# Kernel optimization log

Measured on AMD Instinct MI355X. Metric: run time of the kernel, lower is better.

## Reference

```python
import jax, jax.numpy as jnp
import numpy as np

DIM_U1 = 20
DIM_U2 = 20
DZ = 6
BATCH = 4096


def _mlp(x, Wa, ba, Wb, bb, Wc, bc, Wd, bd):
    h = jax.nn.relu(x @ Wa + ba)
    h = jax.nn.relu(h @ Wb + bb)
    h = jax.nn.relu(h @ Wc + bc)
    return h @ Wd + bd


def setup_inputs() -> dict:
    key = jax.random.key(0)
    ks = jax.random.split(key, 9)

    def lin(k, fan_in, fan_out):
        k1, k2 = jax.random.split(k)
        lim = 1.0 / np.sqrt(fan_in)
        W = jax.random.uniform(k1, (fan_in, fan_out), minval=-lim, maxval=lim, dtype=jnp.float32)
        b = jax.random.uniform(k2, (fan_out,), minval=-lim, maxval=lim, dtype=jnp.float32)
        return W, b

    d = {"x": jax.random.normal(ks[0], (BATCH, DIM_U1), dtype=jnp.float32)}
    dims1 = [(3, 16), (16, 32), (32, 16), (16, 1 + DZ * 3)]
    dims2 = [(3, 16), (16, 32), (32, 16), (16, DZ + 5 * DZ * DZ)]
    names = ["a", "b", "c", "d"]
    for j, (fi, fo) in enumerate(dims1):
        W, b = lin(ks[1 + j], fi, fo)
        d["W1" + names[j]] = W
        d["b1" + names[j]] = b
    for j, (fi, fo) in enumerate(dims2):
        W, b = lin(ks[5 + j], fi, fo)
        d["W2" + names[j]] = W
        d["b2" + names[j]] = b
    return d


def reference(x, W1a, b1a, W1b, b1b, W1c, b1c, W1d, b1d,
              W2a, b2a, W2b, b2b, W2c, b2c, W2d, b2d):
    B = x.shape[0]
    # gather local neighbor triples: [B, dim_u1, 3]
    idx = (jnp.arange(DIM_U1)[:, None] + jnp.arange(-1, 2)[None, :]) % DIM_U1
    xl = x[:, idx]
    out1 = _mlp(xl, W1a, b1a, W1b, b1b, W1c, b1c, W1d, b1d)  # [B, 20, 19]
    out2 = _mlp(xl, W2a, b2a, W2b, b2b, W2c, b2c, W2d, b2d)  # [B, 20, 186]

    f1 = out1[:, :, :1]  # [B, 20, 1]

    # banded scatter for g1: [B, dim_u1, dz*dim_u2]
    rows1 = jnp.arange(DIM_U1)[:, None]
    cols1 = (jnp.arange(3 * DZ)[None, :] + (jnp.arange(DIM_U1)[:, None] - 1) * DZ) % (DZ * DIM_U2)
    g1 = jnp.zeros((B, DIM_U1, DZ * DIM_U2), x.dtype).at[:, rows1, cols1].set(out1[:, :, 1:])

    f2 = out2[:, :, :DZ].reshape(B, DZ * DIM_U2, 1)

    # banded scatter for g2: [B, dz*dim_u2, dz*dim_u2]
    rows2 = jnp.arange(DZ * DIM_U2)[:, None]
    base = (jnp.arange(5 * DZ)[None, :] + (jnp.arange(DIM_U2)[:, None] - 2) * DZ) % (DZ * DIM_U2)  # [20, 30]
    cols2 = jnp.repeat(base, DZ, axis=0)  # [120, 30]
    vals2 = out2[:, :, DZ:].reshape(B, DZ * DIM_U2, 5 * DZ)
    g2 = jnp.zeros((B, DZ * DIM_U2, DZ * DIM_U2), x.dtype).at[:, rows2, cols2].set(vals2)

    return (f1, g1, f2, g2)
```

## Files before the change

kernel.cpp:

```cpp
#include <hip/hip_runtime.h>

#define U 20

struct Ptrs { const float* p[16]; };

__launch_bounds__(64)
__global__ void fused(const float* __restrict__ x, Ptrs pt,
                      float* __restrict__ out, int B, int total) {
    const int tid = threadIdx.x;
    const int t   = blockIdx.x * 64 + tid;

    const size_t g1_off = (size_t)B * 20;
    const size_t f2_off = (size_t)B * 2420;
    const size_t g2_off = (size_t)B * 2540;

    {
        int t0  = blockIdx.x * 64;
        int n_t = total - t0; if (n_t > 64) n_t = 64; if (n_t < 0) n_t = 0;
        float4 z4; z4.x = z4.y = z4.z = z4.w = 0.f;
        float4* z1 = reinterpret_cast<float4*>(out + g1_off + (size_t)t0 * 120);
        int c1 = n_t * 30;
        for (int idx = tid; idx < c1; idx += 64) z1[idx] = z4;
        float4* z2 = reinterpret_cast<float4*>(out + g2_off + (size_t)t0 * 720);
        int c2 = n_t * 180;
        for (int idx = tid; idx < c2; idx += 64) z2[idx] = z4;
    }

    const bool live = (t < total);
    const int b = live ? (t / U) : 0;
    const int i = live ? (t - b * U) : 0;

    const float* W1a = pt.p[0];  const float* b1a = pt.p[1];
    const float* W1b = pt.p[2];  const float* b1b = pt.p[3];
    const float* W1c = pt.p[4];  const float* b1c = pt.p[5];
    const float* W1d = pt.p[6];  const float* b1d = pt.p[7];
    const float* W2a = pt.p[8];  const float* b2a = pt.p[9];
    const float* W2b = pt.p[10]; const float* b2b = pt.p[11];
    const float* W2c = pt.p[12]; const float* b2c = pt.p[13];
    const float* W2d = pt.p[14]; const float* b2d = pt.p[15];

    const float* xb = x + (size_t)b * U;
    int im = (i == 0)     ? U - 1 : i - 1;
    int ip = (i == U - 1) ? 0     : i + 1;
    float v0 = xb[im], v1 = xb[i], v2 = xb[ip];

    float h1[16], h2[32], h3[16];
    float o1[19];

    #pragma unroll
    for (int n = 0; n < 16; n++)
        h1[n] = fmaxf(b1a[n] + v0 * W1a[n] + v1 * W1a[16 + n] + v2 * W1a[32 + n], 0.f);

    #pragma unroll
    for (int n = 0; n < 32; n++) h2[n] = b1b[n];
    #pragma unroll
    for (int k = 0; k < 16; k++) {
        float hk = h1[k];
        #pragma unroll
        for (int n = 0; n < 32; n++) h2[n] += hk * W1b[k * 32 + n];
    }
    #pragma unroll
    for (int n = 0; n < 32; n++) h2[n] = fmaxf(h2[n], 0.f);

    #pragma unroll
    for (int n = 0; n < 16; n++) h3[n] = b1c[n];
    #pragma unroll
    for (int k = 0; k < 32; k++) {
        float hk = h2[k];
        #pragma unroll
        for (int n = 0; n < 16; n++) h3[n] += hk * W1c[k * 16 + n];
    }
    #pragma unroll
    for (int n = 0; n < 16; n++) h3[n] = fmaxf(h3[n], 0.f);

    #pragma unroll
    for (int n = 0; n < 19; n++) o1[n] = b1d[n];
    #pragma unroll
    for (int k = 0; k < 16; k++) {
        float hk = h3[k];
        #pragma unroll
        for (int n = 0; n < 19; n++) o1[n] += hk * W1d[k * 19 + n];
    }

    __syncthreads();
    if (!live) return;

    float* g1row  = out + g1_off + (size_t)t * 120;
    float* g2rows = out + g2_off + (size_t)t * 720;

    out[t] = o1[0];
    #pragma unroll
    for (int j = 0; j < 3; j++) {
        int cc = i - 1 + j;
        if (cc < 0)  cc += U;
        if (cc >= U) cc -= U;
        float2* d = reinterpret_cast<float2*>(g1row + cc * 6);
        #pragma unroll
        for (int m = 0; m < 3; m++) {
            float2 v; v.x = o1[1 + j * 6 + 2 * m]; v.y = o1[1 + j * 6 + 2 * m + 1];
            d[m] = v;
        }
    }

    #pragma unroll
    for (int n = 0; n < 16; n++)
        h1[n] = fmaxf(b2a[n] + v0 * W2a[n] + v1 * W2a[16 + n] + v2 * W2a[32 + n], 0.f);

    #pragma unroll
    for (int n = 0; n < 32; n++) h2[n] = b2b[n];
    #pragma unroll
    for (int k = 0; k < 16; k++) {
        float hk = h1[k];
        #pragma unroll
        for (int n = 0; n < 32; n++) h2[n] += hk * W2b[k * 32 + n];
    }
    #pragma unroll
    for (int n = 0; n < 32; n++) h2[n] = fmaxf(h2[n], 0.f);

    #pragma unroll
    for (int n = 0; n < 16; n++) h3[n] = b2c[n];
    #pragma unroll
    for (int k = 0; k < 32; k++) {
        float hk = h2[k];
        #pragma unroll
        for (int n = 0; n < 16; n++) h3[n] += hk * W2c[k * 16 + n];
    }
    #pragma unroll
    for (int n = 0; n < 16; n++) h3[n] = fmaxf(h3[n], 0.f);

    {
        float o2a[6];
        #pragma unroll
        for (int n = 0; n < 6; n++) o2a[n] = b2d[n];
        #pragma unroll
        for (int k = 0; k < 16; k++) {
            float hk = h3[k];
            #pragma unroll
            for (int n = 0; n < 6; n++) o2a[n] += hk * W2d[k * 186 + n];
        }
        float2* d = reinterpret_cast<float2*>(out + f2_off + (size_t)t * 6);
        #pragma unroll
        for (int m = 0; m < 3; m++) {
            float2 v; v.x = o2a[2 * m]; v.y = o2a[2 * m + 1];
            d[m] = v;
        }
    }

    for (int z = 0; z < 6; z++) {
        float o2[30];
        #pragma unroll
        for (int n = 0; n < 30; n++) o2[n] = b2d[6 + z * 30 + n];
        #pragma unroll
        for (int k = 0; k < 16; k++) {
            float hk = h3[k];
            #pragma unroll
            for (int n = 0; n < 30; n++) o2[n] += hk * W2d[k * 186 + 6 + z * 30 + n];
        }
        float* row = g2rows + z * 120;
        #pragma unroll
        for (int j = 0; j < 5; j++) {
            int cc = i - 2 + j;
            if (cc < 0)  cc += U;
            if (cc >= U) cc -= U;
            float2* d = reinterpret_cast<float2*>(row + cc * 6);
            #pragma unroll
            for (int m = 0; m < 3; m++) {
                float2 v; v.x = o2[j * 6 + 2 * m]; v.y = o2[j * 6 + 2 * m + 1];
                d[m] = v;
            }
        }
    }
}

extern "C" void kernel_launch(void* const* d_in, const int* in_sizes, int n_in,
                              void* d_out, int out_size, void* d_ws, size_t ws_size,
                              hipStream_t stream) {
    const float* x = (const float*)d_in[0];
    Ptrs pt;
    for (int a = 0; a < 16; a++) pt.p[a] = (const float*)d_in[1 + a];

    int total = in_sizes[0];
    int B = total / U;

    int blocks = (total + 63) / 64;
    fused<<<blocks, 64, 0, stream>>>(x, pt, (float*)d_out, B, total);
}
```

Measured before the change: 390.8 us.

## Stage banded outputs in shared memory and write them out coalesced

Instead of zero-filling the global g1/g2 regions and then doing scattered float2 writes per thread, each block builds the full 120-float rows in an LDS tile (zeroed in shared memory) and copies them to global memory with coalesced float4 stores. The same staging is applied to f2. This removes the double write (zero fill plus scatter) to global memory and turns strided writes into contiguous ones. In exchange it adds many __syncthreads barriers and 30KB of LDS per 64-thread block, which may limit occupancy.

```diff
diff --git a/kernel.cpp b/kernel.cpp
--- a/kernel.cpp
+++ b/kernel.cpp
@@ -7,26 +7,17 @@
 __launch_bounds__(64)
 __global__ void fused(const float* __restrict__ x, Ptrs pt,
                       float* __restrict__ out, int B, int total) {
+    __shared__ float buf[64 * 120];
     const int tid = threadIdx.x;
-    const int t   = blockIdx.x * 64 + tid;
+    const int t0  = blockIdx.x * 64;
+    const int t   = t0 + tid;
+    const bool live = (t < total);
+    int n_t = total - t0; if (n_t > 64) n_t = 64; if (n_t < 0) n_t = 0;
 
     const size_t g1_off = (size_t)B * 20;
     const size_t f2_off = (size_t)B * 2420;
     const size_t g2_off = (size_t)B * 2540;
 
-    {
-        int t0  = blockIdx.x * 64;
-        int n_t = total - t0; if (n_t > 64) n_t = 64; if (n_t < 0) n_t = 0;
-        float4 z4; z4.x = z4.y = z4.z = z4.w = 0.f;
-        float4* z1 = reinterpret_cast<float4*>(out + g1_off + (size_t)t0 * 120);
-        int c1 = n_t * 30;
-        for (int idx = tid; idx < c1; idx += 64) z1[idx] = z4;
-        float4* z2 = reinterpret_cast<float4*>(out + g2_off + (size_t)t0 * 720);
-        int c2 = n_t * 180;
-        for (int idx = tid; idx < c2; idx += 64) z2[idx] = z4;
-    }
-
-    const bool live = (t < total);
     const int b = live ? (t / U) : 0;
     const int i = live ? (t - b * U) : 0;
 
@@ -44,8 +35,7 @@
     int ip = (i == U - 1) ? 0     : i + 1;
     float v0 = xb[im], v1 = xb[i], v2 = xb[ip];
 
-    float h1[16], h2[32], h3[16];
-    float o1[19];
+    float h1[16], h2[32], h3[16], o1[19];
 
     #pragma unroll
     for (int n = 0; n < 16; n++)
@@ -82,25 +72,29 @@
         for (int n = 0; n < 19; n++) o1[n] += hk * W1d[k * 19 + n];
     }
 
+    if (live) out[t] = o1[0];
+
+    float4* bv = reinterpret_cast<float4*>(buf);
+    float4 z4; z4.x = z4.y = z4.z = z4.w = 0.f;
+    const int c30 = n_t * 30;
+
+    for (int idx = tid; idx < c30; idx += 64) bv[idx] = z4;
     __syncthreads();
-    if (!live) return;
-
-    float* g1row  = out + g1_off + (size_t)t * 120;
-    float* g2rows = out + g2_off + (size_t)t * 720;
-
-    out[t] = o1[0];
-    #pragma unroll
-    for (int j = 0; j < 3; j++) {
-        int cc = i - 1 + j;
-        if (cc < 0)  cc += U;
-        if (cc >= U) cc -= U;
-        float2* d = reinterpret_cast<float2*>(g1row + cc * 6);
+    if (live) {
+        float* row = buf + tid * 120;
         #pragma unroll
-        for (int m = 0; m < 3; m++) {
-            float2 v; v.x = o1[1 + j * 6 + 2 * m]; v.y = o1[1 + j * 6 + 2 * m + 1];
-            d[m] = v;
+        for (int j = 0; j < 3; j++) {
+            int cc = i - 1 + j; if (cc < 0) cc += U; if (cc >= U) cc -= U;
+            #pragma unroll
+            for (int m = 0; m < 6; m++) row[cc * 6 + m] = o1[1 + j * 6 + m];
         }
     }
+    __syncthreads();
+    {
+        float4* g1v = reinterpret_cast<float4*>(out + g1_off + (size_t)t0 * 120);
+        for (int idx = tid; idx < c30; idx += 64) g1v[idx] = bv[idx];
+    }
+    __syncthreads();
 
     #pragma unroll
     for (int n = 0; n < 16; n++)
@@ -128,7 +122,7 @@
     #pragma unroll
     for (int n = 0; n < 16; n++) h3[n] = fmaxf(h3[n], 0.f);
 
-    {
+    if (live) {
         float o2a[6];
         #pragma unroll
         for (int n = 0; n < 6; n++) o2a[n] = b2d[n];
@@ -138,37 +132,48 @@
             #pragma unroll
             for (int n = 0; n < 6; n++) o2a[n] += hk * W2d[k * 186 + n];
         }
-        float2* d = reinterpret_cast<float2*>(out + f2_off + (size_t)t * 6);
         #pragma unroll
-        for (int m = 0; m < 3; m++) {
-            float2 v; v.x = o2a[2 * m]; v.y = o2a[2 * m + 1];
-            d[m] = v;
-        }
+        for (int n = 0; n < 6; n++) buf[tid * 6 + n] = o2a[n];
     }
+    __syncthreads();
+    {
+        float2* f2g = reinterpret_cast<float2*>(out + f2_off + (size_t)t0 * 6);
+        float2* bv2 = reinterpret_cast<float2*>(buf);
+        int c = n_t * 3;
+        for (int idx = tid; idx < c; idx += 64) f2g[idx] = bv2[idx];
+    }
+    __syncthreads();
 
     for (int z = 0; z < 6; z++) {
-        float o2[30];
-        #pragma unroll
-        for (int n = 0; n < 30; n++) o2[n] = b2d[6 + z * 30 + n];
-        #pragma unroll
-        for (int k = 0; k < 16; k++) {
-            float hk = h3[k];
+        for (int idx = tid; idx < c30; idx += 64) bv[idx] = z4;
+        __syncthreads();
+        if (live) {
+            float o2[30];
             #pragma unroll
-            for (int n = 0; n < 30; n++) o2[n] += hk * W2d[k * 186 + 6 + z * 30 + n];
-        }
-        float* row = g2rows + z * 120;
-        #pragma unroll
-        for (int j = 0; j < 5; j++) {
-            int cc = i - 2 + j;
-            if (cc < 0)  cc += U;
-            if (cc >= U) cc -= U;
-            float2* d = reinterpret_cast<float2*>(row + cc * 6);
+            for (int n = 0; n < 30; n++) o2[n] = b2d[6 + z * 30 + n];
             #pragma unroll
-            for (int m = 0; m < 3; m++) {
-                float2 v; v.x = o2[j * 6 + 2 * m]; v.y = o2[j * 6 + 2 * m + 1];
-                d[m] = v;
+            for (int k = 0; k < 16; k++) {
+                float hk = h3[k];
+                #pragma unroll
+                for (int n = 0; n < 30; n++) o2[n] += hk * W2d[k * 186 + 6 + z * 30 + n];
+            }
+            float* row = buf + tid * 120;
+            #pragma unroll
+            for (int j = 0; j < 5; j++) {
+                int cc = i - 2 + j; if (cc < 0) cc += U; if (cc >= U) cc -= U;
+                #pragma unroll
+                for (int m = 0; m < 6; m++) row[cc * 6 + m] = o2[j * 6 + m];
             }
         }
+        __syncthreads();
+        for (int idx = tid; idx < c30; idx += 64) {
+            int tau = idx / 30;
+            int c   = idx - tau * 30;
+            float4* dst = reinterpret_cast<float4*>(
+                out + g2_off + (size_t)(t0 + tau) * 720 + z * 120 + c * 4);
+            *dst = bv[idx];
+        }
+        __syncthreads();
     }
 }
 
```

New measurement: 391.6 us. Within noise of the previous version (+0.2%).

## Stage MLP weights in LDS and zero output rows per thread

Applied to the files above, without the earlier changes.

All weights and biases are copied into shared memory at block start, with W2d padded to a 188 stride for aligned float2 reads. The hidden layer of width 32 is spilled to a per-thread LDS row instead of registers. The cooperative block-wide zero fill is replaced by each thread zeroing its own g1/g2 rows right before its banded writes. Inner loops are partially rolled to reduce register pressure. This trades repeated global and scalar weight loads for a per-block LDS staging cost of about 23KB plus LDS traffic. The per-thread zero fill gives strided, less coalesced stores and then rewrites the same lines with the banded values.

```diff
diff --git a/kernel.cpp b/kernel.cpp
--- a/kernel.cpp
+++ b/kernel.cpp
@@ -4,172 +4,165 @@
 
 struct Ptrs { const float* p[16]; };
 
+#define W1A 0
+#define B1A 48
+#define W1B 64
+#define B1B 576
+#define W1C 608
+#define B1C 1120
+#define W1D 1136
+#define B1D 1440
+#define W2A 1460
+#define B2A 1508
+#define W2B 1524
+#define B2B 2036
+#define W2C 2068
+#define B2C 2580
+#define W2D 2596
+#define B2D (W2D + 16*188)
+#define NW   5792
+#define H2O  NW
+#define LDSZ (NW + 64*33)
+
 __launch_bounds__(64)
 __global__ void fused(const float* __restrict__ x, Ptrs pt,
                       float* __restrict__ out, int B, int total) {
+    __shared__ float lds[LDSZ];
     const int tid = threadIdx.x;
     const int t   = blockIdx.x * 64 + tid;
+
+    {
+        const int lens[16] = {48,16,512,32,512,16,304,19,48,16,512,32,512,16,2976,186};
+        const int offs[16] = {W1A,B1A,W1B,B1B,W1C,B1C,W1D,B1D,W2A,B2A,W2B,B2B,W2C,B2C,W2D,B2D};
+        for (int a = 0; a < 16; a++) {
+            const float* s = pt.p[a];
+            const int len = lens[a], off = offs[a];
+            if (a == 14) {
+                for (int e = tid; e < len; e += 64) {
+                    int k = e / 186, n = e - k * 186;
+                    lds[off + k * 188 + n] = s[e];
+                }
+            } else {
+                for (int e = tid; e < len; e += 64) lds[off + e] = s[e];
+            }
+        }
+    }
+    __syncthreads();
+    if (t >= total) return;
+
+    const int b = t / U;
+    const int i = t - b * U;
+
+    const float* xb = x + (size_t)b * U;
+    const int im = (i == 0)     ? U - 1 : i - 1;
+    const int ip = (i == U - 1) ? 0     : i + 1;
+    const float v0 = xb[im], v1 = xb[i], v2 = xb[ip];
 
     const size_t g1_off = (size_t)B * 20;
     const size_t f2_off = (size_t)B * 2420;
     const size_t g2_off = (size_t)B * 2540;
+    float* g1row  = out + g1_off + (size_t)t * 120;
+    float* g2rows = out + g2_off + (size_t)t * 720;
+    float* hrow   = lds + H2O + tid * 33;
+
+    float4 z4; z4.x = z4.y = z4.z = z4.w = 0.f;
+    float h1[16], h3[16];
+
+#define TRUNK(wA,bA,wB,bB,wC,bC)                                              \
+    {                                                                         \
+        _Pragma("unroll")                                                     \
+        for (int n = 0; n < 16; n++)                                          \
+            h1[n] = fmaxf(lds[(bA)+n] + v0*lds[(wA)+n] + v1*lds[(wA)+16+n]    \
+                          + v2*lds[(wA)+32+n], 0.f);                          \
+        _Pragma("unroll 1")                                                   \
+        for (int n = 0; n < 32; n += 4) {                                     \
+            float a0 = lds[(bB)+n], a1 = lds[(bB)+n+1];                       \
+            float a2 = lds[(bB)+n+2], a3 = lds[(bB)+n+3];                     \
+            _Pragma("unroll")                                                 \
+            for (int k = 0; k < 16; k++) {                                    \
+                const float4 wv = *reinterpret_cast<const float4*>(           \
+                    &lds[(wB) + k*32 + n]);                                   \
+                a0 += h1[k]*wv.x; a1 += h1[k]*wv.y;                           \
+                a2 += h1[k]*wv.z; a3 += h1[k]*wv.w;                           \
+            }                                                                 \
+            hrow[n]   = fmaxf(a0, 0.f); hrow[n+1] = fmaxf(a1, 0.f);           \
+            hrow[n+2] = fmaxf(a2, 0.f); hrow[n+3] = fmaxf(a3, 0.f);           \
+        }                                                                     \
+        _Pragma("unroll")                                                     \
+        for (int n = 0; n < 16; n++) h3[n] = lds[(bC)+n];                     \
+        _Pragma("unroll 1")                                                   \
+        for (int k = 0; k < 32; k++) {                                        \
+            const float hk = hrow[k];                                         \
+            const float4* wr = reinterpret_cast<const float4*>(               \
+                &lds[(wC) + k*16]);                                           \
+            _Pragma("unroll")                                                 \
+            for (int q = 0; q < 4; q++) {                                     \
+                const float4 wv = wr[q];                                      \
+                h3[4*q]   += hk*wv.x; h3[4*q+1] += hk*wv.y;                   \
+                h3[4*q+2] += hk*wv.z; h3[4*q+3] += hk*wv.w;                   \
+            }                                                                 \
+        }                                                                     \
+        _Pragma("unroll")                                                     \
+        for (int n = 0; n < 16; n++) h3[n] = fmaxf(h3[n], 0.f);               \
+    }
+
+    TRUNK(W1A, B1A, W1B, B1B, W1C, B1C)
 
     {
-        int t0  = blockIdx.x * 64;
-        int n_t = total - t0; if (n_t > 64) n_t = 64; if (n_t < 0) n_t = 0;
-        float4 z4; z4.x = z4.y = z4.z = z4.w = 0.f;
-        float4* z1 = reinterpret_cast<float4*>(out + g1_off + (size_t)t0 * 120);
-        int c1 = n_t * 30;
-        for (int idx = tid; idx < c1; idx += 64) z1[idx] = z4;
-        float4* z2 = reinterpret_cast<float4*>(out + g2_off + (size_t)t0 * 720);
-        int c2 = n_t * 180;
-        for (int idx = tid; idx < c2; idx += 64) z2[idx] = z4;
-    }
-
-    const bool live = (t < total);
-    const int b = live ? (t / U) : 0;
-    const int i = live ? (t - b * U) : 0;
-
-    const float* W1a = pt.p[0];  const float* b1a = pt.p[1];
-    const float* W1b = pt.p[2];  const float* b1b = pt.p[3];
-    const float* W1c = pt.p[4];  const float* b1c = pt.p[5];
-    const float* W1d = pt.p[6];  const float* b1d = pt.p[7];
-    const float* W2a = pt.p[8];  const float* b2a = pt.p[9];
-    const float* W2b = pt.p[10]; const float* b2b = pt.p[11];
-    const float* W2c = pt.p[12]; const float* b2c = pt.p[13];
-    const float* W2d = pt.p[14]; const float* b2d = pt.p[15];
-
-    const float* xb = x + (size_t)b * U;
-    int im = (i == 0)     ? U - 1 : i - 1;
-    int ip = (i == U - 1) ? 0     : i + 1;
-    float v0 = xb[im], v1 = xb[i], v2 = xb[ip];
-
-    float h1[16], h2[32], h3[16];
-    float o1[19];
-
-    #pragma unroll
-    for (int n = 0; n < 16; n++)
-        h1[n] = fmaxf(b1a[n] + v0 * W1a[n] + v1 * W1a[16 + n] + v2 * W1a[32 + n], 0.f);
-
-    #pragma unroll
-    for (int n = 0; n < 32; n++) h2[n] = b1b[n];
-    #pragma unroll
-    for (int k = 0; k < 16; k++) {
-        float hk = h1[k];
+        float4* d = reinterpret_cast<float4*>(g1row);
         #pragma unroll
-        for (int n = 0; n < 32; n++) h2[n] += hk * W1b[k * 32 + n];
-    }
-    #pragma unroll
-    for (int n = 0; n < 32; n++) h2[n] = fmaxf(h2[n], 0.f);
-
-    #pragma unroll
-    for (int n = 0; n < 16; n++) h3[n] = b1c[n];
-    #pragma unroll
-    for (int k = 0; k < 32; k++) {
-        float hk = h2[k];
-        #pragma unroll
-        for (int n = 0; n < 16; n++) h3[n] += hk * W1c[k * 16 + n];
-    }
-    #pragma unroll
-    for (int n = 0; n < 16; n++) h3[n] = fmaxf(h3[n], 0.f);
-
-    #pragma unroll
-    for (int n = 0; n < 19; n++) o1[n] = b1d[n];
-    #pragma unroll
-    for (int k = 0; k < 16; k++) {
-        float hk = h3[k];
-        #pragma unroll
-        for (int n = 0; n < 19; n++) o1[n] += hk * W1d[k * 19 + n];
-    }
-
-    __syncthreads();
-    if (!live) return;
-
-    float* g1row  = out + g1_off + (size_t)t * 120;
-    float* g2rows = out + g2_off + (size_t)t * 720;
-
-    out[t] = o1[0];
-    #pragma unroll
-    for (int j = 0; j < 3; j++) {
-        int cc = i - 1 + j;
-        if (cc < 0)  cc += U;
-        if (cc >= U) cc -= U;
-        float2* d = reinterpret_cast<float2*>(g1row + cc * 6);
-        #pragma unroll
-        for (int m = 0; m < 3; m++) {
-            float2 v; v.x = o1[1 + j * 6 + 2 * m]; v.y = o1[1 + j * 6 + 2 * m + 1];
-            d[m] = v;
+        for (int m = 0; m < 30; m++) d[m] = z4;
+        #pragma unroll 1
+        for (int n = 0; n < 19; n++) {
+            float acc = lds[B1D + n];
+            #pragma unroll
+            for (int k = 0; k < 16; k++) acc += h3[k] * lds[W1D + k*19 + n];
+            if (n == 0) {
+                out[t] = acc;
+            } else {
+                int m = n - 1;
+                int j = m / 6, r = m - j * 6;
+                int cc = i - 1 + j; if (cc < 0) cc += U; if (cc >= U) cc -= U;
+                g1row[cc * 6 + r] = acc;
+            }
         }
     }
 
-    #pragma unroll
-    for (int n = 0; n < 16; n++)
-        h1[n] = fmaxf(b2a[n] + v0 * W2a[n] + v1 * W2a[16 + n] + v2 * W2a[32 + n], 0.f);
+    TRUNK(W2A, B2A, W2B, B2B, W2C, B2C)
 
-    #pragma unroll
-    for (int n = 0; n < 32; n++) h2[n] = b2b[n];
-    #pragma unroll
-    for (int k = 0; k < 16; k++) {
-        float hk = h1[k];
+    #pragma unroll 1
+    for (int n = 0; n < 6; n++) {
+        float acc = lds[B2D + n];
         #pragma unroll
-        for (int n = 0; n < 32; n++) h2[n] += hk * W2b[k * 32 + n];
+        for (int k = 0; k < 16; k++) acc += h3[k] * lds[W2D + k*188 + n];
+        out[f2_off + (size_t)t * 6 + n] = acc;
     }
-    #pragma unroll
-    for (int n = 0; n < 32; n++) h2[n] = fmaxf(h2[n], 0.f);
 
-    #pragma unroll
-    for (int n = 0; n < 16; n++) h3[n] = b2c[n];
-    #pragma unroll
-    for (int k = 0; k < 32; k++) {
-        float hk = h2[k];
+    #pragma unroll 1
+    for (int z = 0; z < 6; z++) {
+        float* row = g2rows + z * 120;
+        float4* rv = reinterpret_cast<float4*>(row);
         #pragma unroll
-        for (int n = 0; n < 16; n++) h3[n] += hk * W2c[k * 16 + n];
-    }
-    #pragma unroll
-    for (int n = 0; n < 16; n++) h3[n] = fmaxf(h3[n], 0.f);
-
-    {
-        float o2a[6];
-        #pragma unroll
-        for (int n = 0; n < 6; n++) o2a[n] = b2d[n];
-        #pragma unroll
-        for (int k = 0; k < 16; k++) {
-            float hk = h3[k];
+        for (int m = 0; m < 30; m++) rv[m] = z4;
+        const int nb = 6 + z * 30;
+        #pragma unroll 1
+        for (int p = 0; p < 15; p++) {
+            const int n = nb + 2 * p;
+            float a0 = lds[B2D + n], a1 = lds[B2D + n + 1];
             #pragma unroll
-            for (int n = 0; n < 6; n++) o2a[n] += hk * W2d[k * 186 + n];
-        }
-        float2* d = reinterpret_cast<float2*>(out + f2_off + (size_t)t * 6);
-        #pragma unroll
-        for (int m = 0; m < 3; m++) {
-            float2 v; v.x = o2a[2 * m]; v.y = o2a[2 * m + 1];
-            d[m] = v;
+            for (int k = 0; k < 16; k++) {
+                const float2 wv = *reinterpret_cast<const float2*>(
+                    &lds[W2D + k*188 + n]);
+                a0 += h3[k] * wv.x; a1 += h3[k] * wv.y;
+            }
+            const int r = 2 * p;
+            const int j = r / 6, m2 = r - j * 6;
+            int cc = i - 2 + j; if (cc < 0) cc += U; if (cc >= U) cc -= U;
+            float2 v; v.x = a0; v.y = a1;
+            *reinterpret_cast<float2*>(row + cc * 6 + m2) = v;
         }
     }
-
-    for (int z = 0; z < 6; z++) {
-        float o2[30];
-        #pragma unroll
-        for (int n = 0; n < 30; n++) o2[n] = b2d[6 + z * 30 + n];
-        #pragma unroll
-        for (int k = 0; k < 16; k++) {
-            float hk = h3[k];
-            #pragma unroll
-            for (int n = 0; n < 30; n++) o2[n] += hk * W2d[k * 186 + 6 + z * 30 + n];
-        }
-        float* row = g2rows + z * 120;
-        #pragma unroll
-        for (int j = 0; j < 5; j++) {
-            int cc = i - 2 + j;
-            if (cc < 0)  cc += U;
-            if (cc >= U) cc -= U;
-            float2* d = reinterpret_cast<float2*>(row + cc * 6);
-            #pragma unroll
-            for (int m = 0; m < 3; m++) {
-                float2 v; v.x = o2[j * 6 + 2 * m]; v.y = o2[j * 6 + 2 * m + 1];
-                d[m] = v;
-            }
-        }
-    }
+#undef TRUNK
 }
 
 extern "C" void kernel_launch(void* const* d_in, const int* in_sizes, int n_in,
```

After: 417.3 us. 1.07x slower.

## Split fused kernel into MLP compute to workspace and banded expand kernel

Applied to the files above, without the earlier changes.

The single fused kernel is split in two. The first computes both MLPs and writes only the compact band values into a workspace buffer. The second launches one thread per output row, zero-fills the row and scatters the band values into place. The aim is to separate the compute-bound MLP from the write-bound zero fill and scatter, so each runs with a better-suited launch shape. The cost is an extra kernel launch and a workspace round trip through global memory, and the expand kernel's per-thread row writes may not coalesce well.

```diff
diff --git a/kernel.cpp b/kernel.cpp
--- a/kernel.cpp
+++ b/kernel.cpp
@@ -5,30 +5,13 @@
 struct Ptrs { const float* p[16]; };
 
 __launch_bounds__(64)
-__global__ void fused(const float* __restrict__ x, Ptrs pt,
-                      float* __restrict__ out, int B, int total) {
-    const int tid = threadIdx.x;
-    const int t   = blockIdx.x * 64 + tid;
-
-    const size_t g1_off = (size_t)B * 20;
-    const size_t f2_off = (size_t)B * 2420;
-    const size_t g2_off = (size_t)B * 2540;
-
-    {
-        int t0  = blockIdx.x * 64;
-        int n_t = total - t0; if (n_t > 64) n_t = 64; if (n_t < 0) n_t = 0;
-        float4 z4; z4.x = z4.y = z4.z = z4.w = 0.f;
-        float4* z1 = reinterpret_cast<float4*>(out + g1_off + (size_t)t0 * 120);
-        int c1 = n_t * 30;
-        for (int idx = tid; idx < c1; idx += 64) z1[idx] = z4;
-        float4* z2 = reinterpret_cast<float4*>(out + g2_off + (size_t)t0 * 720);
-        int c2 = n_t * 180;
-        for (int idx = tid; idx < c2; idx += 64) z2[idx] = z4;
-    }
-
-    const bool live = (t < total);
-    const int b = live ? (t / U) : 0;
-    const int i = live ? (t - b * U) : 0;
+__global__ void mlp_compute(const float* __restrict__ x, Ptrs pt,
+                            float* __restrict__ out, float* __restrict__ ws,
+                            int B, int total) {
+    const int t = blockIdx.x * 64 + threadIdx.x;
+    if (t >= total) return;
+    const int b = t / U;
+    const int i = t - b * U;
 
     const float* W1a = pt.p[0];  const float* b1a = pt.p[1];
     const float* W1b = pt.p[2];  const float* b1b = pt.p[3];
@@ -40,17 +23,15 @@
     const float* W2d = pt.p[14]; const float* b2d = pt.p[15];
 
     const float* xb = x + (size_t)b * U;
-    int im = (i == 0)     ? U - 1 : i - 1;
-    int ip = (i == U - 1) ? 0     : i + 1;
-    float v0 = xb[im], v1 = xb[i], v2 = xb[ip];
+    const int im = (i == 0)     ? U - 1 : i - 1;
+    const int ip = (i == U - 1) ? 0     : i + 1;
+    const float v0 = xb[im], v1 = xb[i], v2 = xb[ip];
 
     float h1[16], h2[32], h3[16];
-    float o1[19];
 
     #pragma unroll
     for (int n = 0; n < 16; n++)
         h1[n] = fmaxf(b1a[n] + v0 * W1a[n] + v1 * W1a[16 + n] + v2 * W1a[32 + n], 0.f);
-
     #pragma unroll
     for (int n = 0; n < 32; n++) h2[n] = b1b[n];
     #pragma unroll
@@ -61,7 +42,6 @@
     }
     #pragma unroll
     for (int n = 0; n < 32; n++) h2[n] = fmaxf(h2[n], 0.f);
-
     #pragma unroll
     for (int n = 0; n < 16; n++) h3[n] = b1c[n];
     #pragma unroll
@@ -72,32 +52,21 @@
     }
     #pragma unroll
     for (int n = 0; n < 16; n++) h3[n] = fmaxf(h3[n], 0.f);
-
-    #pragma unroll
-    for (int n = 0; n < 19; n++) o1[n] = b1d[n];
-    #pragma unroll
-    for (int k = 0; k < 16; k++) {
-        float hk = h3[k];
-        #pragma unroll
-        for (int n = 0; n < 19; n++) o1[n] += hk * W1d[k * 19 + n];
-    }
-
-    __syncthreads();
-    if (!live) return;
-
-    float* g1row  = out + g1_off + (size_t)t * 120;
-    float* g2rows = out + g2_off + (size_t)t * 720;
-
-    out[t] = o1[0];
-    #pragma unroll
-    for (int j = 0; j < 3; j++) {
-        int cc = i - 1 + j;
-        if (cc < 0)  cc += U;
-        if (cc >= U) cc -= U;
-        float2* d = reinterpret_cast<float2*>(g1row + cc * 6);
-        #pragma unroll
-        for (int m = 0; m < 3; m++) {
-            float2 v; v.x = o1[1 + j * 6 + 2 * m]; v.y = o1[1 + j * 6 + 2 * m + 1];
+    {
+        float o1[19];
+        #pragma unroll
+        for (int n = 0; n < 19; n++) o1[n] = b1d[n];
+        #pragma unroll
+        for (int k = 0; k < 16; k++) {
+            float hk = h3[k];
+            #pragma unroll
+            for (int n = 0; n < 19; n++) o1[n] += hk * W1d[k * 19 + n];
+        }
+        out[t] = o1[0];
+        float2* d = reinterpret_cast<float2*>(ws + (size_t)t * 18);
+        #pragma unroll
+        for (int m = 0; m < 9; m++) {
+            float2 v; v.x = o1[1 + 2 * m]; v.y = o1[2 + 2 * m];
             d[m] = v;
         }
     }
@@ -105,7 +74,6 @@
     #pragma unroll
     for (int n = 0; n < 16; n++)
         h1[n] = fmaxf(b2a[n] + v0 * W2a[n] + v1 * W2a[16 + n] + v2 * W2a[32 + n], 0.f);
-
     #pragma unroll
     for (int n = 0; n < 32; n++) h2[n] = b2b[n];
     #pragma unroll
@@ -116,7 +84,6 @@
     }
     #pragma unroll
     for (int n = 0; n < 32; n++) h2[n] = fmaxf(h2[n], 0.f);
-
     #pragma unroll
     for (int n = 0; n < 16; n++) h3[n] = b2c[n];
     #pragma unroll
@@ -129,6 +96,7 @@
     for (int n = 0; n < 16; n++) h3[n] = fmaxf(h3[n], 0.f);
 
     {
+        const size_t f2_off = (size_t)B * 2420;
         float o2a[6];
         #pragma unroll
         for (int n = 0; n < 6; n++) o2a[n] = b2d[n];
@@ -146,6 +114,8 @@
         }
     }
 
+    float* w2dst = ws + (size_t)total * 18 + (size_t)t * 180;
+    #pragma unroll 1
     for (int z = 0; z < 6; z++) {
         float o2[30];
         #pragma unroll
@@ -156,17 +126,58 @@
             #pragma unroll
             for (int n = 0; n < 30; n++) o2[n] += hk * W2d[k * 186 + 6 + z * 30 + n];
         }
-        float* row = g2rows + z * 120;
-        #pragma unroll
-        for (int j = 0; j < 5; j++) {
-            int cc = i - 2 + j;
-            if (cc < 0)  cc += U;
-            if (cc >= U) cc -= U;
+        float2* d = reinterpret_cast<float2*>(w2dst + z * 30);
+        #pragma unroll
+        for (int m = 0; m < 15; m++) {
+            float2 v; v.x = o2[2 * m]; v.y = o2[2 * m + 1];
+            d[m] = v;
+        }
+    }
+}
+
+__launch_bounds__(256)
+__global__ void expand(const float* __restrict__ ws, float* __restrict__ out,
+                       int B, int total) {
+    const int rid = blockIdx.x * 256 + threadIdx.x;
+    const size_t g1_off = (size_t)B * 20;
+    const size_t g2_off = (size_t)B * 2540;
+    float4 z4; z4.x = z4.y = z4.z = z4.w = 0.f;
+
+    if (rid < total) {
+        const int t = rid;
+        const int i = t % U;
+        float* row = out + g1_off + (size_t)t * 120;
+        float4* rv = reinterpret_cast<float4*>(row);
+        #pragma unroll
+        for (int m = 0; m < 30; m++) rv[m] = z4;
+        const float2* src = reinterpret_cast<const float2*>(ws + (size_t)t * 18);
+        #pragma unroll
+        for (int j = 0; j < 3; j++) {
+            int cc = i - 1 + j; if (cc < 0) cc += U; if (cc >= U) cc -= U;
             float2* d = reinterpret_cast<float2*>(row + cc * 6);
-            #pragma unroll
-            for (int m = 0; m < 3; m++) {
-                float2 v; v.x = o2[j * 6 + 2 * m]; v.y = o2[j * 6 + 2 * m + 1];
-                d[m] = v;
+            d[0] = src[j * 3 + 0];
+            d[1] = src[j * 3 + 1];
+            d[2] = src[j * 3 + 2];
+        }
+    } else {
+        const int q = rid - total;
+        if (q < total * 6) {
+            const int t = q / 6;
+            const int z = q - 6 * t;
+            const int i = t % U;
+            float* row = out + g2_off + (size_t)q * 120;
+            float4* rv = reinterpret_cast<float4*>(row);
+            #pragma unroll
+            for (int m = 0; m < 30; m++) rv[m] = z4;
+            const float2* src = reinterpret_cast<const float2*>(
+                ws + (size_t)total * 18 + (size_t)t * 180 + z * 30);
+            #pragma unroll
+            for (int j = 0; j < 5; j++) {
+                int cc = i - 2 + j; if (cc < 0) cc += U; if (cc >= U) cc -= U;
+                float2* d = reinterpret_cast<float2*>(row + cc * 6);
+                d[0] = src[j * 3 + 0];
+                d[1] = src[j * 3 + 1];
+                d[2] = src[j * 3 + 2];
             }
         }
     }
@@ -182,6 +193,12 @@
     int total = in_sizes[0];
     int B = total / U;
 
-    int blocks = (total + 63) / 64;
-    fused<<<blocks, 64, 0, stream>>>(x, pt, (float*)d_out, B, total);
+    int blocksA = (total + 63) / 64;
+    mlp_compute<<<blocksA, 64, 0, stream>>>(x, pt, (float*)d_out, (float*)d_ws,
+                                            B, total);
+
+    int rows = total * 7;
+    int blocksB = (rows + 255) / 256;
+    expand<<<blocksB, 256, 0, stream>>>((const float*)d_ws, (float*)d_out,
+                                        B, total);
 }
```

After: 506.6 us. 1.3x slower.
